# Optimization experiments

Hardware: AMD Instinct MI355X
Metric: run time of the kernel (lower is better)

## Reference

```python
import jax, jax.numpy as jnp
import numpy as np

HEADS = 12
WH = WW = 7
N = WH * WW  # 49 tokens per window
NW = 64      # windows per image (mask groups)


def _relative_position_index():
    ch, cw = np.meshgrid(np.arange(WH), np.arange(WW), indexing='ij')
    coords = np.stack([ch, cw]).reshape(2, -1)  # [2, N]
    rel = coords[:, :, None] - coords[:, None, :]  # [2, N, N]
    rel = rel.transpose(1, 2, 0)
    rel[:, :, 0] += WH - 1
    rel[:, :, 1] += WW - 1
    rel[:, :, 0] *= 2 * WW - 1
    return rel.sum(-1).astype(np.int32)  # [N, N]


def setup_inputs() -> dict:
    key = jax.random.key(0)
    ks = jax.random.split(key, 6)
    B, C = 4096, 384
    x = jax.random.normal(ks[0], (B, N, C), dtype=jnp.float32)
    mask = jnp.where(jax.random.uniform(ks[1], (NW, N, N)) > 0.5, 0.0, -100.0).astype(jnp.float32)
    W_qkv = jax.random.normal(ks[2], (C, 3 * C), dtype=jnp.float32) * 0.02
    b_qkv = jnp.zeros((3 * C,), dtype=jnp.float32)
    W_out = jax.random.normal(ks[3], (C, C), dtype=jnp.float32) * 0.02
    b_out = jnp.zeros((C,), dtype=jnp.float32)
    rpb_table = jax.random.normal(ks[4], ((2 * WH - 1) * (2 * WW - 1), HEADS), dtype=jnp.float32) * 0.01
    rel_index = jnp.asarray(_relative_position_index())
    return {"x": x, "mask": mask, "W_qkv": W_qkv, "b_qkv": b_qkv,
            "W_out": W_out, "b_out": b_out, "rpb_table": rpb_table,
            "rel_index": rel_index}


def reference(x, mask, W_qkv, b_qkv, W_out, b_out, rpb_table, rel_index):
    B, n, C = x.shape
    hd = C // HEADS
    scale = hd ** (-0.5)
    qkv = x @ W_qkv + b_qkv                      # [B, n, 3C]
    q, k, v = jnp.split(qkv, 3, axis=2)
    def heads(t):
        return t.reshape(B, n, HEADS, hd).transpose(0, 2, 1, 3)  # b h n d
    q = heads(q) * scale
    k = heads(k)
    v = heads(v)
    attn = jnp.einsum('bhmc,bhnc->bhmn', q, k)   # [B, h, n, n]
    bias = rpb_table[rel_index.reshape(-1)].reshape(n, n, HEADS).transpose(2, 0, 1)
    attn = attn + bias[None]
    nw = mask.shape[0]
    attn = attn.reshape(B // nw, nw, HEADS, n, n) + mask[None, :, None]
    attn = attn.reshape(B, HEADS, n, n)
    attn = jax.nn.softmax(attn, axis=3)
    out = jnp.einsum('bhmn,bhnc->bhmc', attn, v)  # [B, h, n, d]
    out = out.transpose(0, 2, 1, 3).reshape(B, n, C)
    return out @ W_out + b_out
```

## Files before the change

### kernel.cpp

```cpp
#include <hip/hip_runtime.h>

#define NTOK 49
#define CDIM 384
#define HEADS 12
#define HD 32
#define NWIN 64
#define NQKV 1152
#define SCALE 0.17677669529663687f

typedef __attribute__((ext_vector_type(8))) __bf16 bf16x8;
typedef __attribute__((ext_vector_type(4))) float f32x4;

#define OFF_WQKVT   0ull
#define OFF_WOUTT   884736ull
#define OFF_RPBF    1179648ull
#define OFF_MASKF   1376256ull
#define OFF_QKVB    8555520ull
#define OFF_ATTNOUT 470977536ull
#define OFF_XB      OFF_ATTNOUT

#define TSIZE 77070336ull

__device__ __forceinline__ void async_copy16(__bf16* lds_dst, const __bf16* g_src) {
    __builtin_amdgcn_global_load_lds(
        (const __attribute__((address_space(1))) void*)g_src,
        (__attribute__((address_space(3))) void*)lds_dst,
        16, 0, 0);
}


__global__ void prep_weights(const float* __restrict__ Wqkv, const float* __restrict__ Wout,
                             __bf16* __restrict__ WqkvT, __bf16* __restrict__ WoutT) {
    int idx = blockIdx.x * 256 + threadIdx.x;
    if (idx < NQKV * CDIM) {
        int n = idx / CDIM, k = idx % CDIM;
        WqkvT[idx] = (__bf16)Wqkv[(size_t)k * NQKV + n];
    }
    if (idx < CDIM * CDIM) {
        int n = idx / CDIM, k = idx % CDIM;
        WoutT[idx] = (__bf16)Wout[(size_t)k * CDIM + n];
    }
}

__global__ void prep_frag(const float* __restrict__ rpb, const int* __restrict__ rel,
                          const float* __restrict__ mask,
                          float* __restrict__ rpbF, float* __restrict__ maskF) {
    int idx = blockIdx.x * 256 + threadIdx.x;
    if (idx < 49152) {
        int r = idx & 3, lane = (idx >> 2) & 63, nt = (idx >> 8) & 3, mt = (idx >> 10) & 3, h = idx >> 12;
        int m = mt * 16 + ((lane >> 4) << 2) + r, n = nt * 16 + (lane & 15);
        rpbF[idx] = (m < NTOK && n < NTOK) ? rpb[rel[m * NTOK + n] * HEADS + h] : 0.f;
    } else {
        int i2 = idx - 49152;
        if (i2 < 262144) {
            int r = i2 & 3, lane = (i2 >> 2) & 63, nt = (i2 >> 8) & 3, mt = (i2 >> 10) & 3, w = i2 >> 12;
            int m = mt * 16 + ((lane >> 4) << 2) + r, n = nt * 16 + (lane & 15);
            maskF[i2] = (m < NTOK && n < NTOK) ? mask[(size_t)w * NTOK * NTOK + m * NTOK + n] : 0.f;
        }
    }
}

__global__ __launch_bounds__(256) void prep_xb(const float* __restrict__ x,
                                               __bf16* __restrict__ xb, int total8) {
    int stride = gridDim.x * 256;
    for (int i = blockIdx.x * 256 + threadIdx.x; i < total8; i += stride) {
        float4 a = reinterpret_cast<const float4*>(x)[i * 2];
        float4 b = reinterpret_cast<const float4*>(x)[i * 2 + 1];
        union { __bf16 h[8]; uint4 u; } t;
        t.h[0] = (__bf16)a.x; t.h[1] = (__bf16)a.y; t.h[2] = (__bf16)a.z; t.h[3] = (__bf16)a.w;
        t.h[4] = (__bf16)b.x; t.h[5] = (__bf16)b.y; t.h[6] = (__bf16)b.z; t.h[7] = (__bf16)b.w;
        reinterpret_cast<uint4*>(xb)[i] = t.u;
    }
}


__global__ __launch_bounds__(256, 4) void gemm_qkv(
    const __bf16* __restrict__ xb, const __bf16* __restrict__ WqkvT,
    const float* __restrict__ bqkv, __bf16* __restrict__ qkvb)
{
    __shared__ __attribute__((aligned(16))) __bf16 smem[16384];
    __bf16* As = smem;
    __bf16* Bs = smem + 8192;

    const int cpx  = 14112 >> 3;
    const int lid  = (blockIdx.x & 7) * cpx + (blockIdx.x >> 3);
    const int mblk = lid / 9, nblk = lid % 9;
    const int n0  = nblk * 128;
    const int bm0 = mblk * 128;

    const int tid = threadIdx.x;
    const int wave = tid >> 6, lane = tid & 63;
    const int l15 = lane & 15, l4 = lane >> 4;
    const int wr = wave >> 1, wc = wave & 1;

    f32x4 acc[4][4] = {};

    for (int k0 = 0; k0 < CDIM; k0 += 64) {
#pragma unroll
        for (int j = 0; j < 4; ++j) {
            int c = wave * 4 + j;
            int mt = c >> 1, kk = c & 1;
            const __bf16* sa = xb + (size_t)(bm0 + mt * 16 + l15) * CDIM + k0 + kk * 32 + l4 * 8;
            async_copy16(&As[c * 512], sa);
            const __bf16* sb = WqkvT + (size_t)(n0 + mt * 16 + l15) * CDIM + k0 + kk * 32 + l4 * 8;
            async_copy16(&Bs[c * 512], sb);
        }
        __syncthreads();

#pragma unroll
        for (int kk = 0; kk < 2; ++kk) {
            bf16x8 af[4], bf[4];
#pragma unroll
            for (int mi = 0; mi < 4; ++mi)
                af[mi] = *reinterpret_cast<const bf16x8*>(&As[((wr * 4 + mi) * 2 + kk) * 512 + lane * 8]);
#pragma unroll
            for (int ni = 0; ni < 4; ++ni)
                bf[ni] = *reinterpret_cast<const bf16x8*>(&Bs[((wc * 4 + ni) * 2 + kk) * 512 + lane * 8]);
#pragma unroll
            for (int mi = 0; mi < 4; ++mi)
#pragma unroll
                for (int ni = 0; ni < 4; ++ni)
                    acc[mi][ni] = __builtin_amdgcn_mfma_f32_16x16x32_bf16(af[mi], bf[ni], acc[mi][ni], 0, 0, 0);
        }
        __syncthreads();
    }

    const float scl = (n0 < CDIM) ? SCALE : 1.0f;
    float bias[4];
#pragma unroll
    for (int ni = 0; ni < 4; ++ni)
        bias[ni] = bqkv[n0 + wc * 64 + ni * 16 + l15];

    __bf16* Cs = smem;
#pragma unroll
    for (int mi = 0; mi < 4; ++mi)
#pragma unroll
        for (int ni = 0; ni < 4; ++ni)
#pragma unroll
            for (int r = 0; r < 4; ++r) {
                int row = wr * 64 + mi * 16 + l4 * 4 + r;
                int col = wc * 64 + ni * 16 + l15;
                int byte = (row * 256 + col * 2) ^ (((row >> 2) & 3) << 5);
                *reinterpret_cast<__bf16*>(reinterpret_cast<char*>(Cs) + byte) =
                    (__bf16)((acc[mi][ni][r] + bias[ni]) * scl);
            }
    __syncthreads();

    const int which = n0 / CDIM;
    const int h0    = (n0 % CDIM) >> 5;
    __bf16* tbase = qkvb + (size_t)which * TSIZE;
#pragma unroll
    for (int it = 0; it < 8; ++it) {
        int idx = it * 4096 + tid * 16;
        int row = idx >> 8, bcol = idx & 255;
        int sb = (row * 256 + bcol) ^ (((row >> 2) & 3) << 5);
        uint4 v = *reinterpret_cast<const uint4*>(reinterpret_cast<const char*>(Cs) + sb);
        int grow = bm0 + row;
        int b = grow / NTOK, tok = grow - b * NTOK;
        int col = bcol >> 1;
        int h = h0 + (col >> 5), d = col & 31;
        *reinterpret_cast<uint4*>(&tbase[(((size_t)b * HEADS + h) * NTOK + tok) * HD + d]) = v;
    }
}


__global__ __launch_bounds__(256) void attn(
    const __bf16* __restrict__ qkvb, const float* __restrict__ rpbF,
    const float* __restrict__ maskF, __bf16* __restrict__ attnout)
{
    __shared__ __attribute__((aligned(16))) __bf16 vt[4][32 * 64];
    __shared__ __attribute__((aligned(16))) __bf16 ps[4][2][64][8];
    const int b = blockIdx.x;
    const int tid = threadIdx.x;
    const int wave = tid >> 6, lane = tid & 63;
    const int l15 = lane & 15, l4 = lane >> 4;
    const int h = blockIdx.y * 4 + wave;
    const int w = b & (NWIN - 1);

    const size_t hoff = (((size_t)b * HEADS + h) * NTOK) * HD;
    const __bf16* qb = qkvb + hoff;
    const __bf16* kb = qkvb + TSIZE + hoff;
    const __bf16* vb = qkvb + 2 * TSIZE + hoff;
    const f32x4* rpbF4  = reinterpret_cast<const f32x4*>(rpbF);
    const f32x4* maskF4 = reinterpret_cast<const f32x4*>(maskF);

    {
        const int tokb = lane >> 2;
        const int c8   = (lane & 3) * 8;
#pragma unroll
        for (int i = 0; i < 4; ++i) {
            int tok = i * 16 + tokb;
            bf16x8 vv = *reinterpret_cast<const bf16x8*>(vb + (size_t)tok * HD + c8);
#pragma unroll
            for (int j = 0; j < 8; ++j) {
                int d = c8 + j;
                vt[wave][d * 64 + (tok ^ ((d & 7) << 3))] = vv[j];
            }
        }
    }

    bf16x8 kf[4];
#pragma unroll
    for (int nt = 0; nt < 4; ++nt)
        kf[nt] = *reinterpret_cast<const bf16x8*>(kb + (size_t)(nt * 16 + l15) * HD + l4 * 8);

    for (int mt = 0; mt < 4; ++mt) {
        bf16x8 qf = *reinterpret_cast<const bf16x8*>(qb + (size_t)(mt * 16 + l15) * HD + l4 * 8);

        f32x4 rb[4], mb[4];
#pragma unroll
        for (int nt = 0; nt < 4; ++nt) {
            rb[nt] = rpbF4[((h * 4 + mt) * 4 + nt) * 64 + lane];
            mb[nt] = maskF4[((w * 4 + mt) * 4 + nt) * 64 + lane];
        }

        f32x4 s[4];
#pragma unroll
        for (int nt = 0; nt < 4; ++nt) {
            f32x4 z = {};
            s[nt] = __builtin_amdgcn_mfma_f32_16x16x32_bf16(qf, kf[nt], z, 0, 0, 0);
        }

#pragma unroll
        for (int r = 0; r < 4; ++r) {
            float vals[4];
#pragma unroll
            for (int nt = 0; nt < 4; ++nt) {
                int n = nt * 16 + l15;
                vals[nt] = (n < NTOK) ? (s[nt][r] + rb[nt][r] + mb[nt][r]) : -1e30f;
            }
            float mx = fmaxf(fmaxf(vals[0], vals[1]), fmaxf(vals[2], vals[3]));
            mx = fmaxf(mx, __shfl_xor(mx, 1));
            mx = fmaxf(mx, __shfl_xor(mx, 2));
            mx = fmaxf(mx, __shfl_xor(mx, 4));
            mx = fmaxf(mx, __shfl_xor(mx, 8));
            float e0 = __expf(vals[0] - mx);
            float e1 = __expf(vals[1] - mx);
            float e2 = __expf(vals[2] - mx);
            float e3 = __expf(vals[3] - mx);
            float sum = (e0 + e1) + (e2 + e3);
            sum += __shfl_xor(sum, 1);
            sum += __shfl_xor(sum, 2);
            sum += __shfl_xor(sum, 4);
            sum += __shfl_xor(sum, 8);
            float inv = 1.0f / sum;
            float ev[4] = {e0, e1, e2, e3};
#pragma unroll
            for (int nt = 0; nt < 4; ++nt) {
                int lp = (l4 * 4 + r) + 16 * ((nt & 1) * 2 + (l15 >> 3));
                ps[wave][nt >> 1][lp][l15 & 7] = (__bf16)(ev[nt] * inv);
            }
        }

        f32x4 o[2] = {};
#pragma unroll
        for (int kb2 = 0; kb2 < 2; ++kb2) {
            bf16x8 ap = *reinterpret_cast<const bf16x8*>(&ps[wave][kb2][lane][0]);
#pragma unroll
            for (int dt = 0; dt < 2; ++dt) {
                int d = dt * 16 + l15;
                bf16x8 bv = *reinterpret_cast<const bf16x8*>(
                    &vt[wave][d * 64 + ((kb2 * 32 + l4 * 8) ^ ((l15 & 7) << 3))]);
                o[dt] = __builtin_amdgcn_mfma_f32_16x16x32_bf16(ap, bv, o[dt], 0, 0, 0);
            }
        }
#pragma unroll
        for (int dt = 0; dt < 2; ++dt) {
            int col = h * HD + dt * 16 + l15;
#pragma unroll
            for (int r = 0; r < 4; ++r) {
                int tok = mt * 16 + l4 * 4 + r;
                if (tok < NTOK)
                    attnout[((size_t)b * NTOK + tok) * CDIM + col] = (__bf16)o[dt][r];
            }
        }
    }
}


__global__ __launch_bounds__(256, 3) void out_proj(
    const __bf16* __restrict__ A, const __bf16* __restrict__ WoutT,
    const float* __restrict__ bout, float* __restrict__ out)
{
    __shared__ __attribute__((aligned(16))) __bf16 as[4 * 12 * 512];
    const int blk = blockIdx.x, tid = threadIdx.x;
    const int wave = tid >> 6, lane = tid & 63;
    const int l15 = lane & 15, l4 = lane >> 4;

    const __bf16* Ab = A + (size_t)blk * 64 * CDIM;
    for (int i = tid; i < 64 * CDIM / 8; i += 256) {
        int4 ld = reinterpret_cast<const int4*>(Ab)[i];
        int e = i * 8;
        int row = e / CDIM, c = e % CDIM;
        int mt = row >> 4, kb = c >> 5;
        int lp = (row & 15) + 16 * ((c & 31) >> 3);
        int slot = lp ^ (kb & 7);
        *reinterpret_cast<int4*>(&as[((mt * 12 + kb) * 64 + slot) * 8]) = ld;
    }
    __syncthreads();

    f32x4 acc[6][4] = {};
    for (int kb = 0; kb < 12; ++kb) {
        int slot = lane ^ (kb & 7);
        bf16x8 af[4];
#pragma unroll
        for (int mt = 0; mt < 4; ++mt)
            af[mt] = *reinterpret_cast<const bf16x8*>(&as[((mt * 12 + kb) * 64 + slot) * 8]);
#pragma unroll
        for (int j = 0; j < 6; ++j) {
            int col = (wave * 6 + j) * 16 + l15;
            bf16x8 bf = *reinterpret_cast<const bf16x8*>(WoutT + (size_t)col * CDIM + kb * 32 + l4 * 8);
#pragma unroll
            for (int mt = 0; mt < 4; ++mt)
                acc[j][mt] = __builtin_amdgcn_mfma_f32_16x16x32_bf16(af[mt], bf, acc[j][mt], 0, 0, 0);
        }
    }
#pragma unroll
    for (int j = 0; j < 6; ++j) {
        int col = (wave * 6 + j) * 16 + l15;
        float bias = bout[col];
#pragma unroll
        for (int mt = 0; mt < 4; ++mt) {
#pragma unroll
            for (int r = 0; r < 4; ++r) {
                size_t row = (size_t)blk * 64 + mt * 16 + l4 * 4 + r;
                out[row * CDIM + col] = acc[j][mt][r] + bias;
            }
        }
    }
}


extern "C" void kernel_launch(void* const* d_in, const int* in_sizes, int n_in,
                              void* d_out, int out_size, void* d_ws, size_t ws_size,
                              hipStream_t stream) {
    (void)n_in; (void)out_size; (void)ws_size;
    const float* x    = (const float*)d_in[0];
    const float* mask = (const float*)d_in[1];
    const float* Wqkv = (const float*)d_in[2];
    const float* bqkv = (const float*)d_in[3];
    const float* Wout = (const float*)d_in[4];
    const float* bout = (const float*)d_in[5];
    const float* rpb  = (const float*)d_in[6];
    const int*   rel  = (const int*)d_in[7];

    const int B = in_sizes[0] / (NTOK * CDIM);
    const int M = B * NTOK;

    char* ws = (char*)d_ws;
    __bf16* WqkvT   = (__bf16*)(ws + OFF_WQKVT);
    __bf16* WoutT   = (__bf16*)(ws + OFF_WOUTT);
    float*  rpbF    = (float*)(ws + OFF_RPBF);
    float*  maskF   = (float*)(ws + OFF_MASKF);
    __bf16* qkvb    = (__bf16*)(ws + OFF_QKVB);
    __bf16* xb      = (__bf16*)(ws + OFF_XB);
    __bf16* attnout = (__bf16*)(ws + OFF_ATTNOUT);
    float*  out     = (float*)d_out;

    prep_weights<<<(NQKV * CDIM + 255) / 256, 256, 0, stream>>>(Wqkv, Wout, WqkvT, WoutT);
    prep_frag<<<(49152 + 262144) / 256, 256, 0, stream>>>(rpb, rel, mask, rpbF, maskF);
    prep_xb<<<2048, 256, 0, stream>>>(x, xb, M * CDIM / 8);
    gemm_qkv<<<(M / 128) * (NQKV / 128), 256, 0, stream>>>(xb, WqkvT, bqkv, qkvb);
    attn<<<dim3(B, 3), 256, 0, stream>>>(qkvb, rpbF, maskF, attnout);
    out_proj<<<M / 64, 256, 0, stream>>>(attnout, WoutT, bout, out);
}
```

Measured before the change: 892.0 us.

## Retile output projection as 128x128 LDS-staged GEMM with async copies and block swizzle

The output projection previously loaded a 64-row A tile into LDS and streamed W_out fragments directly from global memory for every k step, with each block covering all 384 columns. It now tiles the output into 128x128 blocks. Both A and W_out slices are staged into LDS through global_load_lds async copies in 64-wide k chunks, and blocks are remapped with an XCD-style swizzle for L2 locality. The aim is better operand reuse and fewer redundant global weight reads, at the cost of extra syncs per k-step and no double buffering. The grid size hardcodes 4704 tiles, so it assumes a fixed M.

```diff
diff --git a/kernel.cpp b/kernel.cpp
--- a/kernel.cpp
+++ b/kernel.cpp
@@ -278,56 +278,72 @@
 }
 
 
-__global__ __launch_bounds__(256, 3) void out_proj(
+__global__ __launch_bounds__(256, 4) void out_proj(
     const __bf16* __restrict__ A, const __bf16* __restrict__ WoutT,
     const float* __restrict__ bout, float* __restrict__ out)
 {
-    __shared__ __attribute__((aligned(16))) __bf16 as[4 * 12 * 512];
-    const int blk = blockIdx.x, tid = threadIdx.x;
+    __shared__ __attribute__((aligned(16))) __bf16 smem[16384];
+    __bf16* As = smem;
+    __bf16* Bs = smem + 8192;
+
+    const int cpx  = 4704 >> 3;
+    const int lid  = (blockIdx.x & 7) * cpx + (blockIdx.x >> 3);
+    const int mblk = lid / 3, nblk = lid % 3;
+    const int n0  = nblk * 128;
+    const int bm0 = mblk * 128;
+
+    const int tid = threadIdx.x;
     const int wave = tid >> 6, lane = tid & 63;
     const int l15 = lane & 15, l4 = lane >> 4;
-
-    const __bf16* Ab = A + (size_t)blk * 64 * CDIM;
-    for (int i = tid; i < 64 * CDIM / 8; i += 256) {
-        int4 ld = reinterpret_cast<const int4*>(Ab)[i];
-        int e = i * 8;
-        int row = e / CDIM, c = e % CDIM;
-        int mt = row >> 4, kb = c >> 5;
-        int lp = (row & 15) + 16 * ((c & 31) >> 3);
-        int slot = lp ^ (kb & 7);
-        *reinterpret_cast<int4*>(&as[((mt * 12 + kb) * 64 + slot) * 8]) = ld;
-    }
-    __syncthreads();
-
-    f32x4 acc[6][4] = {};
-    for (int kb = 0; kb < 12; ++kb) {
-        int slot = lane ^ (kb & 7);
-        bf16x8 af[4];
-#pragma unroll
-        for (int mt = 0; mt < 4; ++mt)
-            af[mt] = *reinterpret_cast<const bf16x8*>(&as[((mt * 12 + kb) * 64 + slot) * 8]);
-#pragma unroll
-        for (int j = 0; j < 6; ++j) {
-            int col = (wave * 6 + j) * 16 + l15;
-            bf16x8 bf = *reinterpret_cast<const bf16x8*>(WoutT + (size_t)col * CDIM + kb * 32 + l4 * 8);
-#pragma unroll
-            for (int mt = 0; mt < 4; ++mt)
-                acc[j][mt] = __builtin_amdgcn_mfma_f32_16x16x32_bf16(af[mt], bf, acc[j][mt], 0, 0, 0);
-        }
-    }
-#pragma unroll
-    for (int j = 0; j < 6; ++j) {
-        int col = (wave * 6 + j) * 16 + l15;
-        float bias = bout[col];
-#pragma unroll
-        for (int mt = 0; mt < 4; ++mt) {
+    const int wr = wave >> 1, wc = wave & 1;
+
+    f32x4 acc[4][4] = {};
+
+    for (int k0 = 0; k0 < CDIM; k0 += 64) {
+#pragma unroll
+        for (int j = 0; j < 4; ++j) {
+            int c = wave * 4 + j;
+            int mt = c >> 1, kk = c & 1;
+            const __bf16* sa = A + (size_t)(bm0 + mt * 16 + l15) * CDIM + k0 + kk * 32 + l4 * 8;
+            async_copy16(&As[c * 512], sa);
+            const __bf16* sb = WoutT + (size_t)(n0 + mt * 16 + l15) * CDIM + k0 + kk * 32 + l4 * 8;
+            async_copy16(&Bs[c * 512], sb);
+        }
+        __syncthreads();
+
+#pragma unroll
+        for (int kk = 0; kk < 2; ++kk) {
+            bf16x8 af[4], bf[4];
+#pragma unroll
+            for (int mi = 0; mi < 4; ++mi)
+                af[mi] = *reinterpret_cast<const bf16x8*>(&As[((wr * 4 + mi) * 2 + kk) * 512 + lane * 8]);
+#pragma unroll
+            for (int ni = 0; ni < 4; ++ni)
+                bf[ni] = *reinterpret_cast<const bf16x8*>(&Bs[((wc * 4 + ni) * 2 + kk) * 512 + lane * 8]);
+#pragma unroll
+            for (int mi = 0; mi < 4; ++mi)
+#pragma unroll
+                for (int ni = 0; ni < 4; ++ni)
+                    acc[mi][ni] = __builtin_amdgcn_mfma_f32_16x16x32_bf16(af[mi], bf[ni], acc[mi][ni], 0, 0, 0);
+        }
+        __syncthreads();
+    }
+
+    float bias[4];
+#pragma unroll
+    for (int ni = 0; ni < 4; ++ni)
+        bias[ni] = bout[n0 + wc * 64 + ni * 16 + l15];
+
+#pragma unroll
+    for (int mi = 0; mi < 4; ++mi)
+#pragma unroll
+        for (int ni = 0; ni < 4; ++ni)
 #pragma unroll
             for (int r = 0; r < 4; ++r) {
-                size_t row = (size_t)blk * 64 + mt * 16 + l4 * 4 + r;
-                out[row * CDIM + col] = acc[j][mt][r] + bias;
-            }
-        }
-    }
+                size_t row = (size_t)bm0 + wr * 64 + mi * 16 + l4 * 4 + r;
+                int col = n0 + wc * 64 + ni * 16 + l15;
+                out[row * CDIM + col] = acc[mi][ni][r] + bias[ni];
+            }
 }
 
 
@@ -362,5 +378,5 @@
     prep_xb<<<2048, 256, 0, stream>>>(x, xb, M * CDIM / 8);
     gemm_qkv<<<(M / 128) * (NQKV / 128), 256, 0, stream>>>(xb, WqkvT, bqkv, qkvb);
     attn<<<dim3(B, 3), 256, 0, stream>>>(qkvb, rpbF, maskF, attnout);
-    out_proj<<<M / 64, 256, 0, stream>>>(attnout, WoutT, bout, out);
-}
+    out_proj<<<(M / 128) * 3, 256, 0, stream>>>(attnout, WoutT, bout, out);
+}
```

Measured after the change: 828.1 us. 1.08x faster.
